# Kernel optimization log

Hardware: AMD Instinct MI355X
Metric: run time of the kernel (lower is better)

The kernel has to match this reference:

```python
import jax, jax.numpy as jnp
import numpy as np

D_MODEL = 1024
N_HEADS = 16
B, T = 4, 2048


def setup_inputs() -> dict:
    key = jax.random.key(0)
    ks = jax.random.split(key, 5)
    s_in = 1.0 / np.sqrt(D_MODEL)
    x = jax.random.normal(ks[0], (B, T, D_MODEL), dtype=jnp.float32)
    W_qkv = jax.random.uniform(ks[1], (D_MODEL, 3 * D_MODEL), jnp.float32, -s_in, s_in)
    b_qkv = jax.random.uniform(ks[2], (3 * D_MODEL,), jnp.float32, -s_in, s_in)
    W_proj = jax.random.uniform(ks[3], (D_MODEL, D_MODEL), jnp.float32, -s_in, s_in)
    b_proj = jax.random.uniform(ks[4], (D_MODEL,), jnp.float32, -s_in, s_in)
    return {"x": x, "W_qkv": W_qkv, "b_qkv": b_qkv, "W_proj": W_proj, "b_proj": b_proj}


def reference(x, W_qkv, b_qkv, W_proj, b_proj):
    b, t, c = x.shape
    hd = c // N_HEADS  # head dim
    qkv = x @ W_qkv + b_qkv                      # [B,T,3C]
    q, k, v = jnp.split(qkv, 3, axis=2)
    # [B,T,C] -> [B,H,T,hd]
    def heads(z):
        return z.reshape(b, t, N_HEADS, hd).transpose(0, 2, 1, 3)
    q, k, v = heads(q), heads(k), heads(v)
    att = jnp.einsum('bhqd,bhkd->bhqk', q, k) * (1.0 / np.sqrt(hd))
    causal = jnp.tril(jnp.ones((t, t), dtype=bool))
    att = jnp.where(causal, att, -jnp.inf)
    att = jax.nn.softmax(att, axis=-1)
    y = jnp.einsum('bhqk,bhkd->bhqd', att, v)    # [B,H,T,hd]
    y = y.transpose(0, 2, 1, 3).reshape(b, t, c)
    return y @ W_proj + b_proj
```

## Files before the change

kernel.cpp:

```cpp
#include <hip/hip_runtime.h>
#include <hip/hip_bf16.h>

typedef __attribute__((ext_vector_type(4))) float f32x4;
typedef __attribute__((ext_vector_type(8))) short s16x8;
typedef __attribute__((ext_vector_type(4))) short s16x4;

#define D_MODEL 1024
#define NH 16
#define HD 64
#define BB 4
#define TT 2048
#define MROWS (BB * TT)
#define QSCALE 0.18033688011112042f

#define MFMA16(a, b, c) __builtin_amdgcn_mfma_f32_16x16x32_bf16(a, b, c, 0, 0, 0)

#if __has_builtin(__builtin_amdgcn_mfma_f32_16x16x16_bf16)
#define PVMFMA(a, b, c) __builtin_amdgcn_mfma_f32_16x16x16_bf16(a, b, c, 0, 0, 0)
#elif __has_builtin(__builtin_amdgcn_mfma_f32_16x16x16bf16_1k)
#define PVMFMA(a, b, c) __builtin_amdgcn_mfma_f32_16x16x16bf16_1k(a, b, c, 0, 0, 0)
#else
static __device__ __forceinline__ f32x4 pv_mfma_asm(s16x4 a, s16x4 b, f32x4 c) {
  asm volatile("v_mfma_f32_16x16x16_bf16 %0, %1, %2, %0\n\ts_nop 7\n\ts_nop 7"
               : "+v"(c)
               : "v"(a), "v"(b));
  return c;
}
#define PVMFMA(a, b, c) pv_mfma_asm(a, b, c)
#endif

#define GLL16(g, l)                                                                   \
  __builtin_amdgcn_global_load_lds((const __attribute__((address_space(1))) void*)(g), \
                                   (__attribute__((address_space(3))) void*)(l), 16, 0, 0)

static __device__ __forceinline__ unsigned short f2bf(float f) {
  unsigned int u = __float_as_uint(f);
  u += 0x7fff + ((u >> 16) & 1);
  return (unsigned short)(u >> 16);
}

__global__ void k_convert(const float* __restrict__ src, short* __restrict__ dst, int n4) {
  int i = blockIdx.x * blockDim.x + threadIdx.x;
  if (i >= n4) return;
  f32x4 v = reinterpret_cast<const f32x4*>(src)[i];
  s16x4 o;
#pragma unroll
  for (int r = 0; r < 4; r++) o[r] = (short)f2bf(v[r]);
  reinterpret_cast<s16x4*>(dst)[i] = o;
}

__global__ void k_transpose(const float* __restrict__ src, short* __restrict__ dst, int K, int N) {
  __shared__ float tile[32][33];
  int n0 = blockIdx.x * 32, k0 = blockIdx.y * 32;
  int tx = threadIdx.x, ty = threadIdx.y;
#pragma unroll
  for (int i = 0; i < 4; i++) tile[ty + i * 8][tx] = src[(size_t)(k0 + ty + i * 8) * N + n0 + tx];
  __syncthreads();
#pragma unroll
  for (int i = 0; i < 4; i++)
    dst[(size_t)(n0 + ty + i * 8) * K + k0 + tx] = (short)f2bf(tile[tx][ty + i * 8]);
}

__global__ __launch_bounds__(512, 2) void k_gemm_qkv(
    const short* __restrict__ A, const short* __restrict__ Bt, const float* __restrict__ bias,
    short* __restrict__ outQ, short* __restrict__ outK, short* __restrict__ outV) {
  const int K = D_MODEL;
  __shared__ __align__(16) short lds_a[2][256 * 64];
  __shared__ __align__(16) short lds_b[2][128 * 64];
  const int tid = threadIdx.x;
  const int m0 = blockIdx.y * 256, n0 = blockIdx.x * 128;
  const int w = tid >> 6, lane = tid & 63;
  const int wm = (w >> 1) * 64, wn = (w & 1) * 64;
  const int lr = lane & 15, lg = lane >> 4;
  const int srow = lane >> 3;
  const int scol = ((lane & 7) ^ srow) * 8;
  const int r7 = lr & 7;

  const short* aGb = A + (size_t)(m0 + w * 32 + srow) * K + scol;
  const short* bGb = Bt + (size_t)(n0 + w * 16 + srow) * K + scol;

#define QSTAGE(bi, kt)                                                \
  {                                                                   \
    GLL16(aGb + (kt), &lds_a[bi][(w * 32) * 64]);                     \
    GLL16(aGb + (size_t)8 * K + (kt), &lds_a[bi][(w * 32 + 8) * 64]); \
    GLL16(aGb + (size_t)16 * K + (kt), &lds_a[bi][(w * 32 + 16) * 64]); \
    GLL16(aGb + (size_t)24 * K + (kt), &lds_a[bi][(w * 32 + 24) * 64]); \
    GLL16(bGb + (kt), &lds_b[bi][(w * 16) * 64]);                     \
    GLL16(bGb + (size_t)8 * K + (kt), &lds_b[bi][(w * 16 + 8) * 64]); \
  }

  f32x4 acc[4][4] = {};
  const int NT = K / 64;
  QSTAGE(0, 0);
  __syncthreads();
  for (int t = 0; t < NT; ++t) {
    const int cur = t & 1;
    if (t + 1 < NT) QSTAGE(cur ^ 1, (t + 1) * 64);
#pragma unroll
    for (int ks = 0; ks < 2; ks++) {
      s16x8 af[4], bfg[4];
#pragma unroll
      for (int i = 0; i < 4; i++)
        af[i] = *(const s16x8*)&lds_a[cur][(wm + i * 16 + lr) * 64 + ((ks * 4 + lg) ^ r7) * 8];
#pragma unroll
      for (int j = 0; j < 4; j++)
        bfg[j] = *(const s16x8*)&lds_b[cur][(wn + j * 16 + lr) * 64 + ((ks * 4 + lg) ^ r7) * 8];
#pragma unroll
      for (int i = 0; i < 4; i++) {
#pragma unroll
        for (int j = 0; j < 4; j++) acc[i][j] = MFMA16(af[i], bfg[j], acc[i][j]);
      }
    }
    __syncthreads();
  }
#undef QSTAGE

#pragma unroll
  for (int j = 0; j < 4; j++) {
    const int ng = n0 + wn + j * 16 + lr;
    const float bv = bias[ng];
#pragma unroll
    for (int i = 0; i < 4; i++) {
      const int mg = m0 + wm + i * 16 + 4 * lg;
      const int sec = ng >> 10, c = ng & 1023, h = c >> 6, d = c & 63;
      const int b = mg >> 11, t = mg & 2047;
      const int bh = b * NH + h;
      if (sec == 2) {
        s16x4 pk;
#pragma unroll
        for (int r = 0; r < 4; r++) pk[r] = (short)f2bf(acc[i][j][r] + bv);
        *(s16x4*)&outV[((size_t)bh * HD + d) * TT + t] = pk;
      } else {
        short* dst = (sec == 0) ? outQ : outK;
        const float sc = (sec == 0) ? QSCALE : 1.0f;
#pragma unroll
        for (int r = 0; r < 4; r++)
          dst[((size_t)bh * TT + t + r) * HD + d] = (short)f2bf((acc[i][j][r] + bv) * sc);
      }
    }
  }
}

__global__ __launch_bounds__(256, 3) void k_gemm_proj(
    const short* __restrict__ A, const short* __restrict__ Bt, const float* __restrict__ bias,
    float* __restrict__ outF) {
  const int K = D_MODEL, N = D_MODEL;
  __shared__ __align__(16) short lds_a[3][128 * 32];
  __shared__ __align__(16) short lds_b[3][128 * 32];
  const int tid = threadIdx.x;
  const int m0 = blockIdx.y * 128, n0 = blockIdx.x * 128;
  const int w = tid >> 6, lane = tid & 63;
  const int wm = (w >> 1) * 64, wn = (w & 1) * 64;
  const int lr = lane & 15, lg = lane >> 4;

  const short* aG = A + (size_t)(m0 + w * 32 + (lane >> 2)) * K + (lane & 3) * 8;
  const short* bG = Bt + (size_t)(n0 + w * 32 + (lane >> 2)) * K + (lane & 3) * 8;

#define GSTAGE(bi, kt)                                                 \
  {                                                                    \
    GLL16(aG + (kt), &lds_a[bi][(w * 32) * 32]);                       \
    GLL16(aG + (size_t)16 * K + (kt), &lds_a[bi][(w * 32 + 16) * 32]); \
    GLL16(bG + (kt), &lds_b[bi][(w * 32) * 32]);                       \
    GLL16(bG + (size_t)16 * K + (kt), &lds_b[bi][(w * 32 + 16) * 32]); \
  }

  f32x4 acc[4][4] = {};
  const int NT = K / 32;
  GSTAGE(0, 0);
  GSTAGE(1, 32);
  asm volatile("s_waitcnt vmcnt(4)" ::: "memory");
  __builtin_amdgcn_s_barrier();
  __builtin_amdgcn_sched_barrier(0);
  int cur = 0, nx2 = 2;
  for (int t = 0; t < NT; ++t) {
    if (t + 2 < NT) GSTAGE(nx2, (t + 2) * 32);
    s16x8 af[4], bfg[4];
#pragma unroll
    for (int i = 0; i < 4; i++)
      af[i] = *(const s16x8*)&lds_a[cur][(wm + i * 16 + lr) * 32 + lg * 8];
#pragma unroll
    for (int j = 0; j < 4; j++)
      bfg[j] = *(const s16x8*)&lds_b[cur][(wn + j * 16 + lr) * 32 + lg * 8];
#pragma unroll
    for (int i = 0; i < 4; i++) {
#pragma unroll
      for (int j = 0; j < 4; j++) acc[i][j] = MFMA16(af[i], bfg[j], acc[i][j]);
    }
    if (t + 2 < NT) {
      asm volatile("s_waitcnt vmcnt(4) lgkmcnt(0)" ::: "memory");
      __builtin_amdgcn_s_barrier();
      __builtin_amdgcn_sched_barrier(0);
    } else if (t + 1 < NT) {
      asm volatile("s_waitcnt vmcnt(0) lgkmcnt(0)" ::: "memory");
      __builtin_amdgcn_s_barrier();
      __builtin_amdgcn_sched_barrier(0);
    }
    cur = (cur == 2) ? 0 : cur + 1;
    nx2 = (nx2 == 2) ? 0 : nx2 + 1;
  }
#undef GSTAGE

#pragma unroll
  for (int j = 0; j < 4; j++) {
    const int ng = n0 + wn + j * 16 + lr;
    const float bv = bias[ng];
#pragma unroll
    for (int i = 0; i < 4; i++) {
      const int mg = m0 + wm + i * 16 + 4 * lg;
#pragma unroll
      for (int r = 0; r < 4; r++) outF[(size_t)(mg + r) * N + ng] = acc[i][j][r] + bv;
    }
  }
}

__global__ __launch_bounds__(256, 4) void k_attn(const short* __restrict__ Q,
                                                 const short* __restrict__ Kb,
                                                 const short* __restrict__ Vt,
                                                 short* __restrict__ Y) {
  __shared__ __align__(16) short kls[2][64 * 64];
  __shared__ __align__(16) short vls[2][64 * 64];
  const int tid = threadIdx.x, w = tid >> 6, lane = tid & 63;
  const int lr = lane & 15, lg = lane >> 4;
  const int p = blockIdx.x + 16 * blockIdx.y;
  const int xcd = p & 7, idx = p >> 3;
  const int bh = xcd * 8 + (idx >> 4);
  const int xq = idx & 15;
  const int b = bh >> 4, h = bh & 15;
  const short* Qh = Q + (size_t)bh * TT * HD;
  const short* Kh = Kb + (size_t)bh * TT * HD;
  const short* Vh = Vt + (size_t)bh * HD * TT;
  const int srow = lane >> 3;
  const int scol = ((lane & 7) ^ srow) * 8;
  const int r7 = lr & 7;
  const s16x4 vone = {(short)0x3F80, (short)0x3F80, (short)0x3F80, (short)0x3F80};

#define STAGE(bi, kv0)                                                   \
  {                                                                      \
    const short* ks_ = Kh + (size_t)((kv0) + w * 16 + srow) * HD + scol; \
    GLL16(ks_, &kls[bi][(w * 16) * 64]);                                 \
    GLL16(ks_ + 8 * HD, &kls[bi][(w * 16 + 8) * 64]);                    \
    const short* vs_ = Vh + (size_t)(w * 16 + srow) * TT + (kv0) + scol; \
    GLL16(vs_, &vls[bi][(w * 16) * 64]);                                 \
    GLL16(vs_ + 8 * TT, &vls[bi][(w * 16 + 8) * 64]);                    \
  }

#pragma unroll
  for (int ph = 0; ph < 2; ph++) {
    const int panel = ph ? (31 - xq) : xq;
    const int q0w = panel * 64 + w * 16;
    s16x8 qf[2];
#pragma unroll
    for (int kc = 0; kc < 2; kc++)
      qf[kc] = *(const s16x8*)&Qh[(q0w + lr) * HD + kc * 32 + lg * 8];

    f32x4 sacc = {0.f, 0.f, 0.f, 0.f};
    f32x4 oacc[4] = {};

    const int nt = panel + 1;
    STAGE(0, 0);
    __syncthreads();
    for (int t = 0; t < nt; ++t) {
      const int cur = t & 1;
      if (t + 1 < nt) STAGE(cur ^ 1, (t + 1) * 64);
      const int kv0 = t * 64;
      s16x8 kf[4][2];
#pragma unroll
      for (int jk = 0; jk < 4; jk++)
#pragma unroll
        for (int kc = 0; kc < 2; kc++)
          kf[jk][kc] = *(const s16x8*)&kls[cur][(jk * 16 + lr) * 64 + ((kc * 4 + lg) ^ r7) * 8];
      f32x4 s[4] = {};
#pragma unroll
      for (int kc = 0; kc < 2; kc++)
#pragma unroll
        for (int jk = 0; jk < 4; jk++) s[jk] = MFMA16(kf[jk][kc], qf[kc], s[jk]);

      const bool diag = (kv0 + 63 > q0w);
      const int qg = q0w + lr;
      s16x4 pf16[4];
#pragma unroll
      for (int jk = 0; jk < 4; jk++) {
#pragma unroll
        for (int r = 0; r < 4; r++) {
          float pp = exp2f(s[jk][r]);
          if (diag) {
            const int kvg = kv0 + jk * 16 + 4 * lg + r;
            pp = (kvg <= qg) ? pp : 0.f;
          }
          pf16[jk][r] = (short)((__float_as_uint(pp) + 0x8000) >> 16);
        }
      }
#pragma unroll
      for (int jk = 0; jk < 4; jk++) {
        s16x4 vreg[4];
#pragma unroll
        for (int jd = 0; jd < 4; jd++)
          vreg[jd] = *(const s16x4*)&vls[cur][(jd * 16 + lr) * 64 +
                                              ((2 * jk + (lg >> 1)) ^ r7) * 8 + (lg & 1) * 4];
        sacc = PVMFMA(vone, pf16[jk], sacc);
#pragma unroll
        for (int jd = 0; jd < 4; jd++) oacc[jd] = PVMFMA(vreg[jd], pf16[jk], oacc[jd]);
      }
      __syncthreads();
    }
    const float inv = 1.0f / sacc[0];
    const int trow = q0w + lr;
#pragma unroll
    for (int jd = 0; jd < 4; jd++) {
      s16x4 pk;
#pragma unroll
      for (int r = 0; r < 4; r++) pk[r] = (short)f2bf(oacc[jd][r] * inv);
      *(s16x4*)&Y[((size_t)(b * TT + trow)) * D_MODEL + h * HD + jd * 16 + 4 * lg] = pk;
    }
  }
#undef STAGE
}

extern "C" void kernel_launch(void* const* d_in, const int* in_sizes, int n_in,
                              void* d_out, int out_size, void* d_ws, size_t ws_size,
                              hipStream_t stream) {
  const float* x = (const float*)d_in[0];
  const float* Wqkv = (const float*)d_in[1];
  const float* bqkv = (const float*)d_in[2];
  const float* Wproj = (const float*)d_in[3];
  const float* bproj = (const float*)d_in[4];
  float* out = (float*)d_out;

  char* ws = (char*)d_ws;
  short* Xb = (short*)ws;
  short* Wqkvt = (short*)(ws + (16u << 20));
  short* Wprojt = (short*)(ws + (22u << 20));
  short* Qb = (short*)(ws + (24u << 20));
  short* Kb = (short*)(ws + (40u << 20));
  short* Vtb = (short*)(ws + (56u << 20));
  short* Yb = Xb;

  k_convert<<<dim3(MROWS * D_MODEL / 4 / 256), 256, 0, stream>>>(x, Xb, MROWS * D_MODEL / 4);
  k_transpose<<<dim3(3 * D_MODEL / 32, D_MODEL / 32), dim3(32, 8), 0, stream>>>(
      Wqkv, Wqkvt, D_MODEL, 3 * D_MODEL);
  k_transpose<<<dim3(D_MODEL / 32, D_MODEL / 32), dim3(32, 8), 0, stream>>>(
      Wproj, Wprojt, D_MODEL, D_MODEL);
  k_gemm_qkv<<<dim3(3 * D_MODEL / 128, MROWS / 256), 512, 0, stream>>>(
      Xb, Wqkvt, bqkv, Qb, Kb, Vtb);
  k_attn<<<dim3(16, BB * NH), 256, 0, stream>>>(Qb, Kb, Vtb, Yb);
  k_gemm_proj<<<dim3(D_MODEL / 128, MROWS / 128), 256, 0, stream>>>(
      Yb, Wprojt, bproj, out);
}
```

Measured before the change: 289.7 us.

## Enlarge attention query panels to 128 rows and retile projection GEMM to 256x128

The attention kernel now gives each wave 32 query rows (two 16-row groups) that share each staged K/V tile, which halves the number of K/V LDS loads per query and halves the grid. The projection GEMM adopts the QKV GEMM's structure: 512 threads, 256x128 tiles, BK=64 with XOR-swizzled LDS and double buffering instead of triple buffering. Together these aim to raise arithmetic intensity per byte of LDS and global traffic. In exchange, register pressure goes up (attention occupancy is lowered to 3 blocks per CU), there are fewer blocks to spread across CUs, and each causal panel does more wasted masked work on the diagonal.

```diff
diff --git a/kernel.cpp b/kernel.cpp
--- a/kernel.cpp
+++ b/kernel.cpp
@@ -79,14 +79,14 @@
   const short* aGb = A + (size_t)(m0 + w * 32 + srow) * K + scol;
   const short* bGb = Bt + (size_t)(n0 + w * 16 + srow) * K + scol;
 
-#define QSTAGE(bi, kt)                                                \
-  {                                                                   \
-    GLL16(aGb + (kt), &lds_a[bi][(w * 32) * 64]);                     \
-    GLL16(aGb + (size_t)8 * K + (kt), &lds_a[bi][(w * 32 + 8) * 64]); \
+#define QSTAGE(bi, kt)                                                  \
+  {                                                                     \
+    GLL16(aGb + (kt), &lds_a[bi][(w * 32) * 64]);                       \
+    GLL16(aGb + (size_t)8 * K + (kt), &lds_a[bi][(w * 32 + 8) * 64]);   \
     GLL16(aGb + (size_t)16 * K + (kt), &lds_a[bi][(w * 32 + 16) * 64]); \
     GLL16(aGb + (size_t)24 * K + (kt), &lds_a[bi][(w * 32 + 24) * 64]); \
-    GLL16(bGb + (kt), &lds_b[bi][(w * 16) * 64]);                     \
-    GLL16(bGb + (size_t)8 * K + (kt), &lds_b[bi][(w * 16 + 8) * 64]); \
+    GLL16(bGb + (kt), &lds_b[bi][(w * 16) * 64]);                       \
+    GLL16(bGb + (size_t)8 * K + (kt), &lds_b[bi][(w * 16 + 8) * 64]);   \
   }
 
   f32x4 acc[4][4] = {};
@@ -141,64 +141,59 @@
   }
 }
 
-__global__ __launch_bounds__(256, 3) void k_gemm_proj(
+__global__ __launch_bounds__(512, 2) void k_gemm_proj(
     const short* __restrict__ A, const short* __restrict__ Bt, const float* __restrict__ bias,
     float* __restrict__ outF) {
   const int K = D_MODEL, N = D_MODEL;
-  __shared__ __align__(16) short lds_a[3][128 * 32];
-  __shared__ __align__(16) short lds_b[3][128 * 32];
+  __shared__ __align__(16) short lds_a[2][256 * 64];
+  __shared__ __align__(16) short lds_b[2][128 * 64];
   const int tid = threadIdx.x;
-  const int m0 = blockIdx.y * 128, n0 = blockIdx.x * 128;
+  const int m0 = blockIdx.y * 256, n0 = blockIdx.x * 128;
   const int w = tid >> 6, lane = tid & 63;
   const int wm = (w >> 1) * 64, wn = (w & 1) * 64;
   const int lr = lane & 15, lg = lane >> 4;
-
-  const short* aG = A + (size_t)(m0 + w * 32 + (lane >> 2)) * K + (lane & 3) * 8;
-  const short* bG = Bt + (size_t)(n0 + w * 32 + (lane >> 2)) * K + (lane & 3) * 8;
-
-#define GSTAGE(bi, kt)                                                 \
-  {                                                                    \
-    GLL16(aG + (kt), &lds_a[bi][(w * 32) * 32]);                       \
-    GLL16(aG + (size_t)16 * K + (kt), &lds_a[bi][(w * 32 + 16) * 32]); \
-    GLL16(bG + (kt), &lds_b[bi][(w * 32) * 32]);                       \
-    GLL16(bG + (size_t)16 * K + (kt), &lds_b[bi][(w * 32 + 16) * 32]); \
+  const int srow = lane >> 3;
+  const int scol = ((lane & 7) ^ srow) * 8;
+  const int r7 = lr & 7;
+
+  const short* aGb = A + (size_t)(m0 + w * 32 + srow) * K + scol;
+  const short* bGb = Bt + (size_t)(n0 + w * 16 + srow) * K + scol;
+
+#define PSTAGE(bi, kt)                                                  \
+  {                                                                     \
+    GLL16(aGb + (kt), &lds_a[bi][(w * 32) * 64]);                       \
+    GLL16(aGb + (size_t)8 * K + (kt), &lds_a[bi][(w * 32 + 8) * 64]);   \
+    GLL16(aGb + (size_t)16 * K + (kt), &lds_a[bi][(w * 32 + 16) * 64]); \
+    GLL16(aGb + (size_t)24 * K + (kt), &lds_a[bi][(w * 32 + 24) * 64]); \
+    GLL16(bGb + (kt), &lds_b[bi][(w * 16) * 64]);                       \
+    GLL16(bGb + (size_t)8 * K + (kt), &lds_b[bi][(w * 16 + 8) * 64]);   \
   }
 
   f32x4 acc[4][4] = {};
-  const int NT = K / 32;
-  GSTAGE(0, 0);
-  GSTAGE(1, 32);
-  asm volatile("s_waitcnt vmcnt(4)" ::: "memory");
-  __builtin_amdgcn_s_barrier();
-  __builtin_amdgcn_sched_barrier(0);
-  int cur = 0, nx2 = 2;
+  const int NT = K / 64;
+  PSTAGE(0, 0);
+  __syncthreads();
   for (int t = 0; t < NT; ++t) {
-    if (t + 2 < NT) GSTAGE(nx2, (t + 2) * 32);
-    s16x8 af[4], bfg[4];
-#pragma unroll
-    for (int i = 0; i < 4; i++)
-      af[i] = *(const s16x8*)&lds_a[cur][(wm + i * 16 + lr) * 32 + lg * 8];
-#pragma unroll
-    for (int j = 0; j < 4; j++)
-      bfg[j] = *(const s16x8*)&lds_b[cur][(wn + j * 16 + lr) * 32 + lg * 8];
-#pragma unroll
-    for (int i = 0; i < 4; i++) {
-#pragma unroll
-      for (int j = 0; j < 4; j++) acc[i][j] = MFMA16(af[i], bfg[j], acc[i][j]);
-    }
-    if (t + 2 < NT) {
-      asm volatile("s_waitcnt vmcnt(4) lgkmcnt(0)" ::: "memory");
-      __builtin_amdgcn_s_barrier();
-      __builtin_amdgcn_sched_barrier(0);
-    } else if (t + 1 < NT) {
-      asm volatile("s_waitcnt vmcnt(0) lgkmcnt(0)" ::: "memory");
-      __builtin_amdgcn_s_barrier();
-      __builtin_amdgcn_sched_barrier(0);
-    }
-    cur = (cur == 2) ? 0 : cur + 1;
-    nx2 = (nx2 == 2) ? 0 : nx2 + 1;
-  }
-#undef GSTAGE
+    const int cur = t & 1;
+    if (t + 1 < NT) PSTAGE(cur ^ 1, (t + 1) * 64);
+#pragma unroll
+    for (int ks = 0; ks < 2; ks++) {
+      s16x8 af[4], bfg[4];
+#pragma unroll
+      for (int i = 0; i < 4; i++)
+        af[i] = *(const s16x8*)&lds_a[cur][(wm + i * 16 + lr) * 64 + ((ks * 4 + lg) ^ r7) * 8];
+#pragma unroll
+      for (int j = 0; j < 4; j++)
+        bfg[j] = *(const s16x8*)&lds_b[cur][(wn + j * 16 + lr) * 64 + ((ks * 4 + lg) ^ r7) * 8];
+#pragma unroll
+      for (int i = 0; i < 4; i++) {
+#pragma unroll
+        for (int j = 0; j < 4; j++) acc[i][j] = MFMA16(af[i], bfg[j], acc[i][j]);
+      }
+    }
+    __syncthreads();
+  }
+#undef PSTAGE
 
 #pragma unroll
   for (int j = 0; j < 4; j++) {
@@ -213,7 +208,7 @@
   }
 }
 
-__global__ __launch_bounds__(256, 4) void k_attn(const short* __restrict__ Q,
+__global__ __launch_bounds__(256, 3) void k_attn(const short* __restrict__ Q,
                                                  const short* __restrict__ Kb,
                                                  const short* __restrict__ Vt,
                                                  short* __restrict__ Y) {
@@ -221,10 +216,10 @@
   __shared__ __align__(16) short vls[2][64 * 64];
   const int tid = threadIdx.x, w = tid >> 6, lane = tid & 63;
   const int lr = lane & 15, lg = lane >> 4;
-  const int p = blockIdx.x + 16 * blockIdx.y;
+  const int p = blockIdx.x + 8 * blockIdx.y;
   const int xcd = p & 7, idx = p >> 3;
-  const int bh = xcd * 8 + (idx >> 4);
-  const int xq = idx & 15;
+  const int bh = xcd * 8 + (idx >> 3);
+  const int xq = idx & 7;
   const int b = bh >> 4, h = bh & 15;
   const short* Qh = Q + (size_t)bh * TT * HD;
   const short* Kh = Kb + (size_t)bh * TT * HD;
@@ -246,17 +241,19 @@
 
 #pragma unroll
   for (int ph = 0; ph < 2; ph++) {
-    const int panel = ph ? (31 - xq) : xq;
-    const int q0w = panel * 64 + w * 16;
-    s16x8 qf[2];
-#pragma unroll
-    for (int kc = 0; kc < 2; kc++)
-      qf[kc] = *(const s16x8*)&Qh[(q0w + lr) * HD + kc * 32 + lg * 8];
-
-    f32x4 sacc = {0.f, 0.f, 0.f, 0.f};
-    f32x4 oacc[4] = {};
-
-    const int nt = panel + 1;
+    const int panel = ph ? (15 - xq) : xq;
+    const int q0w = panel * 128 + w * 32;
+    s16x8 qf[2][2];
+#pragma unroll
+    for (int jq = 0; jq < 2; jq++)
+#pragma unroll
+      for (int kc = 0; kc < 2; kc++)
+        qf[jq][kc] = *(const s16x8*)&Qh[(q0w + jq * 16 + lr) * HD + kc * 32 + lg * 8];
+
+    f32x4 sacc[2] = {};
+    f32x4 oacc[2][4] = {};
+
+    const int nt = 2 * panel + 2;
     STAGE(0, 0);
     __syncthreads();
     for (int t = 0; t < nt; ++t) {
@@ -269,25 +266,27 @@
 #pragma unroll
         for (int kc = 0; kc < 2; kc++)
           kf[jk][kc] = *(const s16x8*)&kls[cur][(jk * 16 + lr) * 64 + ((kc * 4 + lg) ^ r7) * 8];
-      f32x4 s[4] = {};
-#pragma unroll
-      for (int kc = 0; kc < 2; kc++)
-#pragma unroll
-        for (int jk = 0; jk < 4; jk++) s[jk] = MFMA16(kf[jk][kc], qf[kc], s[jk]);
-
-      const bool diag = (kv0 + 63 > q0w);
-      const int qg = q0w + lr;
-      s16x4 pf16[4];
-#pragma unroll
-      for (int jk = 0; jk < 4; jk++) {
-#pragma unroll
-        for (int r = 0; r < 4; r++) {
-          float pp = exp2f(s[jk][r]);
-          if (diag) {
-            const int kvg = kv0 + jk * 16 + 4 * lg + r;
-            pp = (kvg <= qg) ? pp : 0.f;
+      s16x4 pf16[2][4];
+#pragma unroll
+      for (int jq = 0; jq < 2; jq++) {
+        f32x4 s[4] = {};
+#pragma unroll
+        for (int kc = 0; kc < 2; kc++)
+#pragma unroll
+          for (int jk = 0; jk < 4; jk++) s[jk] = MFMA16(kf[jk][kc], qf[jq][kc], s[jk]);
+        const bool diag = (kv0 + 63 > q0w + jq * 16);
+        const int qg = q0w + jq * 16 + lr;
+#pragma unroll
+        for (int jk = 0; jk < 4; jk++) {
+#pragma unroll
+          for (int r = 0; r < 4; r++) {
+            float pp = exp2f(s[jk][r]);
+            if (diag) {
+              const int kvg = kv0 + jk * 16 + 4 * lg + r;
+              pp = (kvg <= qg) ? pp : 0.f;
+            }
+            pf16[jq][jk][r] = (short)((__float_as_uint(pp) + 0x8000) >> 16);
           }
-          pf16[jk][r] = (short)((__float_as_uint(pp) + 0x8000) >> 16);
         }
       }
 #pragma unroll
@@ -297,20 +296,27 @@
         for (int jd = 0; jd < 4; jd++)
           vreg[jd] = *(const s16x4*)&vls[cur][(jd * 16 + lr) * 64 +
                                               ((2 * jk + (lg >> 1)) ^ r7) * 8 + (lg & 1) * 4];
-        sacc = PVMFMA(vone, pf16[jk], sacc);
-#pragma unroll
-        for (int jd = 0; jd < 4; jd++) oacc[jd] = PVMFMA(vreg[jd], pf16[jk], oacc[jd]);
+#pragma unroll
+        for (int jq = 0; jq < 2; jq++) {
+          sacc[jq] = PVMFMA(vone, pf16[jq][jk], sacc[jq]);
+#pragma unroll
+          for (int jd = 0; jd < 4; jd++)
+            oacc[jq][jd] = PVMFMA(vreg[jd], pf16[jq][jk], oacc[jq][jd]);
+        }
       }
       __syncthreads();
     }
-    const float inv = 1.0f / sacc[0];
-    const int trow = q0w + lr;
-#pragma unroll
-    for (int jd = 0; jd < 4; jd++) {
-      s16x4 pk;
-#pragma unroll
-      for (int r = 0; r < 4; r++) pk[r] = (short)f2bf(oacc[jd][r] * inv);
-      *(s16x4*)&Y[((size_t)(b * TT + trow)) * D_MODEL + h * HD + jd * 16 + 4 * lg] = pk;
+#pragma unroll
+    for (int jq = 0; jq < 2; jq++) {
+      const float inv = 1.0f / sacc[jq][0];
+      const int trow = q0w + jq * 16 + lr;
+#pragma unroll
+      for (int jd = 0; jd < 4; jd++) {
+        s16x4 pk;
+#pragma unroll
+        for (int r = 0; r < 4; r++) pk[r] = (short)f2bf(oacc[jq][jd][r] * inv);
+        *(s16x4*)&Y[((size_t)(b * TT + trow)) * D_MODEL + h * HD + jd * 16 + 4 * lg] = pk;
+      }
     }
   }
 #undef STAGE
@@ -342,7 +348,7 @@
       Wproj, Wprojt, D_MODEL, D_MODEL);
   k_gemm_qkv<<<dim3(3 * D_MODEL / 128, MROWS / 256), 512, 0, stream>>>(
       Xb, Wqkvt, bqkv, Qb, Kb, Vtb);
-  k_attn<<<dim3(16, BB * NH), 256, 0, stream>>>(Qb, Kb, Vtb, Yb);
-  k_gemm_proj<<<dim3(D_MODEL / 128, MROWS / 128), 256, 0, stream>>>(
+  k_attn<<<dim3(8, BB * NH), 256, 0, stream>>>(Qb, Kb, Vtb, Yb);
+  k_gemm_proj<<<dim3(D_MODEL / 128, MROWS / 256), 512, 0, stream>>>(
       Yb, Wprojt, bproj, out);
 }
```

After: 307.6 us. 6.2% more time.
